# Optimization experiments

Hardware: AMD Instinct MI355X
Metric: run time of the kernel (lower is better)

The kernel has to match this reference:

```python
import jax, jax.numpy as jnp
import numpy as np

NEG_SLOPE = 0.2

def gat_conv(x, src, dst, W, a_src, a_dst, b, num_nodes, concat):
    # PyG GATConv (add_self_loops already applied to src/dst).
    H, C = a_src.shape
    h = (x @ W).reshape(-1, H, C)                      # [N,H,C]
    s = jnp.einsum('nhc,hc->nh', h, a_src)             # per-node src score
    d = jnp.einsum('nhc,hc->nh', h, a_dst)             # per-node dst score
    e = jax.nn.leaky_relu(s[src] + d[dst], NEG_SLOPE)  # [E,H]
    emax = jax.lax.stop_gradient(
        jax.ops.segment_max(e, dst, num_segments=num_nodes))  # [N,H]
    ex = jnp.exp(e - emax[dst])
    denom = jax.ops.segment_sum(ex, dst, num_segments=num_nodes)
    alpha = ex / denom[dst]                            # segment softmax over in-edges
    msg = h[src] * alpha[:, :, None]                   # [E,H,C]
    out = jax.ops.segment_sum(msg, dst, num_segments=num_nodes)
    out = out.reshape(num_nodes, H * C) if concat else out.mean(axis=1)
    return out + b

def setup_inputs() -> dict:
    key = jax.random.key(0)
    ks = jax.random.split(key, 20)
    N, E, F = 50000, 400000, 256
    x = jax.random.normal(ks[0], (N, F), dtype=jnp.float32)
    edge_index = jax.random.randint(ks[1], (2, E), 0, N, dtype=jnp.int64)
    def p(k, shape):
        return (jax.random.normal(k, shape, dtype=jnp.float32) * 0.1)
    inp = {'x': x, 'edge_index': edge_index}
    # conv1: 256 -> 8x32 ; conv2: 256 -> 4x32 ; conv3: 128 -> 2x32 ; conv4: 64 -> 1x32
    dims = [(256, 8, 32), (256, 4, 32), (128, 2, 32), (64, 1, 32)]
    ki = 2
    for i, (fin, H, C) in enumerate(dims, start=1):
        inp[f'W{i}'] = p(ks[ki], (fin, H * C)); ki += 1
        inp[f'a_src{i}'] = p(ks[ki], (H, C)); ki += 1
        inp[f'a_dst{i}'] = p(ks[ki], (H, C)); ki += 1
        bdim = H * C if i < 4 else C
        inp[f'b{i}'] = jnp.zeros((bdim,), dtype=jnp.float32)
    return inp

def reference(x, edge_index, W1, a_src1, a_dst1, b1, W2, a_src2, a_dst2, b2,
              W3, a_src3, a_dst3, b3, W4, a_src4, a_dst4, b4):
    N = x.shape[0]
    loops = jnp.arange(N, dtype=edge_index.dtype)
    src = jnp.concatenate([edge_index[0], loops])
    dst = jnp.concatenate([edge_index[1], loops])
    h = jax.nn.elu(gat_conv(x, src, dst, W1, a_src1, a_dst1, b1, N, True))
    h = jax.nn.elu(gat_conv(h, src, dst, W2, a_src2, a_dst2, b2, N, True))
    h = gat_conv(h, src, dst, W3, a_src3, a_dst3, b3, N, True)
    h = jax.nn.elu(h)
    h = gat_conv(h, src, dst, W4, a_src4, a_dst4, b4, N, False)
    return jax.nn.log_softmax(h, axis=1)
```

## Files before the change

kernel.cpp:

```cpp
#include <hip/hip_runtime.h>
#include <hip/hip_bf16.h>

#define LRELU_SLOPE 0.2f

typedef __attribute__((ext_vector_type(8))) short short8;
typedef __attribute__((ext_vector_type(4))) float f32x4;

__device__ __forceinline__ unsigned short bf16r(float f) {
    unsigned int u = __builtin_bit_cast(unsigned int, f);
    u += 0x7fffu + ((u >> 16) & 1u);
    return (unsigned short)(u >> 16);
}
__device__ __forceinline__ float bf2f(unsigned short u) {
    return __builtin_bit_cast(float, (unsigned int)u << 16);
}

#define GLD16(g, l)                                                            \
    __builtin_amdgcn_global_load_lds(                                          \
        (const __attribute__((address_space(1))) void*)(g),                    \
        (__attribute__((address_space(3))) void*)(l), 16, 0, 0)


#define WTOT 108544

__global__ void k_pre(const float* __restrict__ x, unsigned short* __restrict__ Xb,
                      const float* __restrict__ Wa, const float* __restrict__ Wb,
                      const float* __restrict__ Wc, const float* __restrict__ Wd,
                      unsigned short* __restrict__ Ta, unsigned short* __restrict__ Tb,
                      unsigned short* __restrict__ Tc, unsigned short* __restrict__ Td,
                      const int* __restrict__ ei, int* __restrict__ cnt,
                      int* __restrict__ slot, int XC, int E) {
    int gid = blockIdx.x * blockDim.x + threadIdx.x;
    if (gid < XC) {
        const float4* xp = (const float4*)x + (long)gid * 2;
        float4 a = xp[0], b = xp[1];
        short8 pk;
        pk[0] = (short)bf16r(a.x); pk[1] = (short)bf16r(a.y);
        pk[2] = (short)bf16r(a.z); pk[3] = (short)bf16r(a.w);
        pk[4] = (short)bf16r(b.x); pk[5] = (short)bf16r(b.y);
        pk[6] = (short)bf16r(b.z); pk[7] = (short)bf16r(b.w);
        *(short8*)(Xb + (long)gid * 8) = pk;
        return;
    }
    int id = gid - XC;
    if (id < WTOT) {
        const float* W; unsigned short* T; int K, Nc;
        if (id < 65536)       { W = Wa; T = Ta; K = 256; Nc = 256; }
        else if (id < 98304)  { id -= 65536;  W = Wb; T = Tb; K = 256; Nc = 128; }
        else if (id < 106496) { id -= 98304;  W = Wc; T = Tc; K = 128; Nc = 64; }
        else                  { id -= 106496; W = Wd; T = Td; K = 64;  Nc = 32; }
        int n = id / K, k = id % K;
        T[id] = bf16r(W[(long)k * Nc + n]);
        return;
    }
    int e = id - WTOT;
    if (e >= E) return;
    int dst = ei[E + e];
    slot[e] = atomicAdd(&cnt[dst], 1);
}


__global__ void k_scan_blk(const int* __restrict__ cnt, int* __restrict__ offsR,
                           int* __restrict__ bsum, int* __restrict__ bpre,
                           int* __restrict__ done, int N, int NB) {
    __shared__ int temp[1024];
    __shared__ int last_s;
    int t = threadIdx.x;
    int gi = blockIdx.x * 1024 + t;
    int v = (gi < N) ? cnt[gi] + 1 : 0;
    temp[t] = v;
    __syncthreads();
    for (int o = 1; o < 1024; o <<= 1) {
        int x = (t >= o) ? temp[t - o] : 0;
        __syncthreads();
        temp[t] += x;
        __syncthreads();
    }
    if (gi < N) offsR[gi] = temp[t] - v;
    if (t == 1023) bsum[blockIdx.x] = temp[1023];
    if (t == 0) {
        __threadfence();
        last_s = (atomicAdd(done, 1) == NB - 1) ? 1 : 0;
    }
    __syncthreads();
    if (last_s) {
        __threadfence();
        int v2 = (t < NB) ? bsum[t] : 0;
        temp[t] = v2;
        __syncthreads();
        for (int o = 1; o < 1024; o <<= 1) {
            int x = (t >= o) ? temp[t - o] : 0;
            __syncthreads();
            temp[t] += x;
            __syncthreads();
        }
        if (t < NB) bpre[t] = temp[t] - v2;
        if (t == NB - 1) bpre[NB] = temp[t];
    }
}


__global__ void k_finalize(const int* __restrict__ ei, const int* __restrict__ offsR,
                           const int* __restrict__ bpre, const int* __restrict__ slot,
                           int* __restrict__ offs, int* __restrict__ adj,
                           int N, int NB, int E) {
    int gi = blockIdx.x * blockDim.x + threadIdx.x;
    int NA = (N + 256) & ~255;
    if (gi < NA) {
        if (gi < N) {
            int v = offsR[gi] + bpre[gi >> 10];
            offs[gi] = v;
            adj[v] = gi;
        } else if (gi == N) {
            offs[N] = bpre[NB];
        }
        return;
    }
    int e = gi - NA;
    if (e >= E) return;
    int srcn = ei[e];
    int dst  = ei[E + e];
    adj[offsR[dst] + bpre[dst >> 10] + 1 + slot[e]] = srcn;
}


template<int BN, int KT, int GX>
__global__ __launch_bounds__(256) void k_mgemm(const unsigned short* __restrict__ Ab,
                                               const unsigned short* __restrict__ WT,
                                               unsigned short* __restrict__ Cb,
                                               const float* __restrict__ a_src,
                                               const float* __restrict__ a_dst,
                                               float* __restrict__ sbuf,
                                               float* __restrict__ dbuf,
                                               int M, int Nc, int H, int RB) {
    constexpr int KH   = (KT == 256) ? 128 : KT;
    constexpr int NR   = KT / KH;
    constexpr int KITER = KH / 32;
    constexpr int NBF = BN / 16;
    constexpr int CPR = BN / 32;
    constexpr int SP  = BN + 8;
    constexpr int ASH = 64 * KH;
    constexpr int BSH = BN * KH;
    constexpr int EPIL = 64 * SP;
    constexpr int LBSZ = (ASH + BSH) > EPIL ? (ASH + BSH) : EPIL;
    constexpr int CHR = KH / 8;
    constexpr int SHC = (KH == 128) ? 4 : 3;
    constexpr int AIT = CHR / 4;
    constexpr int BIT = BN * CHR / 256;
    __shared__ __align__(16) unsigned short LB[LBSZ];

    int id = blockIdx.x;
    int xcd = id & 7;
    int q  = id >> 3;
    int ct = q % GX;
    int rb = (q / GX) * 8 + xcd;
    if (rb >= RB) return;
    int bm = rb * 64, bn = ct * BN;

    int t = threadIdx.x;
    int wv = t >> 6, l = t & 63;
    int row_in = l & 15, quad = l >> 4;
    char* LBb = (char*)LB;

    const char* Agb = (const char*)Ab;
    const char* WTb = (const char*)WT;

    f32x4 acc[NBF];
#pragma unroll
    for (int j = 0; j < NBF; ++j) acc[j] = (f32x4){0.f, 0.f, 0.f, 0.f};

    int arow = wv * 16 + row_in;

#pragma unroll
    for (int r = 0; r < NR; ++r) {
        if (r > 0) __syncthreads();

#pragma unroll
        for (int i = 0; i < AIT; ++i) {
            int c = i * 256 + t;
            int row = c >> SHC;
            int ci  = c & (CHR - 1);
            int cis = ci ^ (row & 7);
            int grow = bm + row; if (grow >= M) grow = M - 1;
            long gb = (long)grow * (KT * 2) + r * (KH * 2) + cis * 16;
            GLD16(Agb + gb, LBb + (i * 256 + wv * 64) * 16);
        }
#pragma unroll
        for (int i = 0; i < BIT; ++i) {
            int c = i * 256 + t;
            int col = c >> SHC;
            int ci  = c & (CHR - 1);
            int cis = ci ^ (col & 7);
            long gb = (long)(bn + col) * (KT * 2) + r * (KH * 2) + cis * 16;
            GLD16(WTb + gb, LBb + ASH * 2 + (i * 256 + wv * 64) * 16);
        }
        asm volatile("s_waitcnt vmcnt(0)" ::: "memory");
        __syncthreads();

#pragma unroll
        for (int ki = 0; ki < KITER; ++ki) {
            int aoff = (arow * (KH * 2) + ki * 64 + quad * 16) ^ ((arow & 7) << 4);
            short8 av = *(const short8*)(LBb + aoff);
#pragma unroll
            for (int f = 0; f < NBF; ++f) {
                int bcol = f * 16 + row_in;
                int boff = ASH * 2 + ((bcol * (KH * 2) + ki * 64 + quad * 16) ^ ((bcol & 7) << 4));
                short8 bv = *(const short8*)(LBb + boff);
                acc[f] = __builtin_amdgcn_mfma_f32_16x16x32_bf16(av, bv, acc[f], 0, 0, 0);
            }
        }
    }
    __syncthreads();

#pragma unroll
    for (int r = 0; r < 4; ++r)
#pragma unroll
        for (int f = 0; f < NBF; ++f)
            LB[(wv * 16 + quad * 4 + r) * SP + f * 16 + row_in] = bf16r(acc[f][r]);
    __syncthreads();

    int rr = t / CPR, cc = t % CPR;
    if (rr < 64) {
        int grow = bm + rr;
        int colb = bn + cc * 32;
        if (grow < M && colb < Nc) {
            const unsigned short* ep = &LB[rr * SP + cc * 32];
            short8 v0 = *(const short8*)(ep);
            short8 v1 = *(const short8*)(ep + 8);
            short8 v2 = *(const short8*)(ep + 16);
            short8 v3 = *(const short8*)(ep + 24);
            unsigned short* cp = &Cb[(long)grow * Nc + colb];
            *(short8*)(cp)      = v0;
            *(short8*)(cp + 8)  = v1;
            *(short8*)(cp + 16) = v2;
            *(short8*)(cp + 24) = v3;
            int hd = colb >> 5;
            const float* ap = a_src + hd * 32;
            const float* dp = a_dst + hd * 32;
            float ss = 0.f, dd = 0.f;
#pragma unroll
            for (int u = 0; u < 8; ++u) {
                float va = bf2f((unsigned short)v0[u]); ss += va * ap[u];      dd += va * dp[u];
                float vb = bf2f((unsigned short)v1[u]); ss += vb * ap[8 + u];  dd += vb * dp[8 + u];
                float vc = bf2f((unsigned short)v2[u]); ss += vc * ap[16 + u]; dd += vc * dp[16 + u];
                float vd = bf2f((unsigned short)v3[u]); ss += vd * ap[24 + u]; dd += vd * dp[24 + u];
            }
            sbuf[(long)grow * H + hd] = ss;
            dbuf[(long)grow * H + hd] = dd;
        }
    }
}


#define QB(v, k) __builtin_amdgcn_ds_swizzle((v), 0x8000 | ((k) * 0x55))

template<int ACT>
__global__ void k_aggf(const unsigned short* __restrict__ h, const float* __restrict__ s,
                       const float* __restrict__ dsc, const int* __restrict__ offs,
                       const int* __restrict__ adj, const float* __restrict__ bias,
                       unsigned short* __restrict__ out16, float* __restrict__ out32,
                       int N, int H) {
    const int C8 = 4;
    long tid = (long)blockIdx.x * blockDim.x + threadIdx.x;
    int HC8 = H * C8;
    if (tid >= (long)N * HC8) return;
    int c8 = (int)(tid % C8);
    int hh = (int)((tid / C8) % H);
    int n  = (int)(tid / HC8);
    int beg = offs[n], end = offs[n + 1];
    float dn = dsc[n * H + hh];
    int HC = HC8 * 8;
    int coff = hh * 32 + c8 * 8;
    const unsigned short* hb = h + coff;

    float denom = 0.f;
    float acc[8];
#pragma unroll
    for (int u = 0; u < 8; ++u) acc[u] = 0.f;

    for (int j = beg; j < end; j += 4) {
        int my = j + c8;
        int idx = my < end ? my : end - 1;
        int sn = adj[idx];
        float e = s[sn * H + hh] + dn;
        e = e > 0.f ? e : LRELU_SLOPE * e;
        float w = __expf(fminf(e, 80.f));
        if (my >= end) w = 0.f;
        int wi = __builtin_bit_cast(int, w);
        int sn0 = QB(sn, 0);
        int sn1 = QB(sn, 1);
        int sn2 = QB(sn, 2);
        int sn3 = QB(sn, 3);
        float w0 = __builtin_bit_cast(float, QB(wi, 0));
        float w1 = __builtin_bit_cast(float, QB(wi, 1));
        float w2 = __builtin_bit_cast(float, QB(wi, 2));
        float w3 = __builtin_bit_cast(float, QB(wi, 3));
        short8 h0 = *(const short8*)(hb + (size_t)sn0 * HC);
        short8 h1 = *(const short8*)(hb + (size_t)sn1 * HC);
        short8 h2 = *(const short8*)(hb + (size_t)sn2 * HC);
        short8 h3 = *(const short8*)(hb + (size_t)sn3 * HC);
        denom += (w0 + w1) + (w2 + w3);
#pragma unroll
        for (int u = 0; u < 8; ++u) {
            float a01 = w0 * bf2f((unsigned short)h0[u]) + w1 * bf2f((unsigned short)h1[u]);
            float a23 = w2 * bf2f((unsigned short)h2[u]) + w3 * bf2f((unsigned short)h3[u]);
            acc[u] += a01 + a23;
        }
    }

    float inv = 1.0f / denom;
    float o[8];
#pragma unroll
    for (int u = 0; u < 8; ++u) o[u] = acc[u] * inv + bias[coff + u];

    if (ACT == 1) {
        short8 pk;
#pragma unroll
        for (int u = 0; u < 8; ++u) {
            float v = o[u] > 0.f ? o[u] : (__expf(o[u]) - 1.f);
            pk[u] = (short)bf16r(v);
        }
        *(short8*)(out16 + tid * 8) = pk;
    } else {
        float m = o[0];
#pragma unroll
        for (int u = 1; u < 8; ++u) m = fmaxf(m, o[u]);
        m = fmaxf(m, __shfl_xor(m, 1));
        m = fmaxf(m, __shfl_xor(m, 2));
        float ssum = 0.f;
#pragma unroll
        for (int u = 0; u < 8; ++u) ssum += __expf(o[u] - m);
        ssum += __shfl_xor(ssum, 1);
        ssum += __shfl_xor(ssum, 2);
        float lse = m + __logf(ssum);
        float4 lo = {o[0] - lse, o[1] - lse, o[2] - lse, o[3] - lse};
        float4 hi = {o[4] - lse, o[5] - lse, o[6] - lse, o[7] - lse};
        *(float4*)(out32 + tid * 8)     = lo;
        *(float4*)(out32 + tid * 8 + 4) = hi;
    }
}


static inline size_t align_up(size_t x) { return (x + 255) & ~(size_t)255; }

extern "C" void kernel_launch(void* const* d_in, const int* in_sizes, int n_in,
                              void* d_out, int out_size, void* d_ws, size_t ws_size,
                              hipStream_t stream) {
    const float* x   = (const float*)d_in[0];
    const int*   ei  = (const int*)d_in[1];

    const int N = in_sizes[0] / 256;
    const int E = in_sizes[1] / 2;
    const int ET = E + N;
    const int NB = (N + 1023) / 1024;
    const int XC = N * 32;

    size_t off = 0;
    char* ws = (char*)d_ws;
    auto take = [&](size_t bytes) { char* p = ws + off; off += align_up(bytes); return p; };
    int*   offs  = (int*)take((size_t)(N + 1) * 4);
    int*   offsR = (int*)take((size_t)(N + 1) * 4);
    int*   cntd  = (int*)take((size_t)(N + 1) * 4);
    int*   slot  = (int*)take((size_t)E * 4);
    int*   adj   = (int*)take((size_t)ET * 4);
    int*   bsum  = (int*)take((size_t)(NB + 1) * 4);
    int*   bpre  = (int*)take((size_t)(NB + 1) * 4);
    float* sbuf  = (float*)take((size_t)N * 8 * 4);
    float* dbuf  = (float*)take((size_t)N * 8 * 4);
    unsigned short* Xb = (unsigned short*)take((size_t)N * 256 * 2);
    unsigned short* Yb = (unsigned short*)take((size_t)N * 256 * 2);
    unsigned short* WT0 = (unsigned short*)take((size_t)256 * 256 * 2);
    unsigned short* WT1 = (unsigned short*)take((size_t)256 * 128 * 2);
    unsigned short* WT2 = (unsigned short*)take((size_t)128 * 64 * 2);
    unsigned short* WT3 = (unsigned short*)take((size_t)64 * 32 * 2);
    (void)ws_size;

    int* cnt  = cntd;
    int* done = cntd + N;

    hipMemsetAsync(cntd, 0, (size_t)(N + 1) * 4, stream);
    {
        long tot = (long)XC + WTOT + E;
        k_pre<<<(int)((tot + 255) / 256), 256, 0, stream>>>(
            x, Xb,
            (const float*)d_in[2], (const float*)d_in[6], (const float*)d_in[10],
            (const float*)d_in[14], WT0, WT1, WT2, WT3, ei, cnt, slot, XC, E);
        k_scan_blk<<<NB, 1024, 0, stream>>>(cnt, offsR, bsum, bpre, done, N, NB);
        int NA = (N + 256) & ~255;
        k_finalize<<<(NA + E + 255) / 256, 256, 0, stream>>>(
            ei, offsR, bpre, slot, offs, adj, N, NB, E);
    }

    const float* as_[4] = {(const float*)d_in[3], (const float*)d_in[7],
                           (const float*)d_in[11], (const float*)d_in[15]};
    const float* ad_[4] = {(const float*)d_in[4], (const float*)d_in[8],
                           (const float*)d_in[12], (const float*)d_in[16]};
    const float* b_[4]  = {(const float*)d_in[5], (const float*)d_in[9],
                           (const float*)d_in[13], (const float*)d_in[17]};
    int H_[4] = {8, 4, 2, 1};

    const int RB  = (N + 63) / 64;
    const int RBp = ((RB + 7) / 8) * 8;

    for (int li = 0; li < 4; ++li) {
        int H = H_[li];

        if (li == 0) {
            k_mgemm<64, 256, 4><<<4 * RBp, 256, 0, stream>>>(
                Xb, WT0, Yb, as_[0], ad_[0], sbuf, dbuf, N, 256, H, RB);
        } else if (li == 1) {
            k_mgemm<64, 256, 2><<<2 * RBp, 256, 0, stream>>>(
                Xb, WT1, Yb, as_[1], ad_[1], sbuf, dbuf, N, 128, H, RB);
        } else if (li == 2) {
            k_mgemm<64, 128, 1><<<RBp, 256, 0, stream>>>(
                Xb, WT2, Yb, as_[2], ad_[2], sbuf, dbuf, N, 64, H, RB);
        } else {
            k_mgemm<32, 64, 1><<<RBp, 256, 0, stream>>>(
                Xb, WT3, Yb, as_[3], ad_[3], sbuf, dbuf, N, 32, H, RB);
        }
        {
            long total = (long)N * H * 4;
            int nb = (int)((total + 255) / 256);
            if (li < 3)
                k_aggf<1><<<nb, 256, 0, stream>>>(Yb, sbuf, dbuf, offs, adj, b_[li],
                                                  Xb, nullptr, N, H);
            else
                k_aggf<0><<<nb, 256, 0, stream>>>(Yb, sbuf, dbuf, offs, adj, b_[li],
                                                  nullptr, (float*)d_out, N, H);
        }
    }
}
```

Baseline: 294.8 us.

## Fuse aggregation with next-layer GEMM per row block and fold CSR finalize into first GEMM

Replaces the per-layer sequence of separate GEMM and aggregation kernels with fused kernels. Each 64-node row block gathers neighbours, applies the softmax weights, bias and ELU, stages the result in LDS and immediately multiplies it by the next layer's weights. The CSR finalize step is merged into the first GEMM through a grid-stride prologue, and the gather loop now processes 8 edges per iteration. The aim is to remove the global round trip of the intermediate activations and several kernel launches. In exchange the aggregation runs on far fewer threads per launch (one block per 64 rows) and uses more LDS, which can reduce latency hiding for the gather.

```diff
diff --git a/kernel.cpp b/kernel.cpp
--- a/kernel.cpp
+++ b/kernel.cpp
@@ -2,6 +2,7 @@
 #include <hip/hip_bf16.h>
 
 #define LRELU_SLOPE 0.2f
+#define WTOT 108544
 
 typedef __attribute__((ext_vector_type(8))) short short8;
 typedef __attribute__((ext_vector_type(4))) float f32x4;
@@ -20,8 +21,8 @@
         (const __attribute__((address_space(1))) void*)(g),                    \
         (__attribute__((address_space(3))) void*)(l), 16, 0, 0)
 
-
-#define WTOT 108544
+#define QB(v, k) __builtin_amdgcn_ds_swizzle((v), 0x8000 | ((k) * 0x55))
+
 
 __global__ void k_pre(const float* __restrict__ x, unsigned short* __restrict__ Xb,
                       const float* __restrict__ Wa, const float* __restrict__ Wb,
@@ -100,54 +101,48 @@
 }
 
 
-__global__ void k_finalize(const int* __restrict__ ei, const int* __restrict__ offsR,
-                           const int* __restrict__ bpre, const int* __restrict__ slot,
-                           int* __restrict__ offs, int* __restrict__ adj,
-                           int N, int NB, int E) {
-    int gi = blockIdx.x * blockDim.x + threadIdx.x;
-    int NA = (N + 256) & ~255;
-    if (gi < NA) {
-        if (gi < N) {
-            int v = offsR[gi] + bpre[gi >> 10];
-            offs[gi] = v;
-            adj[v] = gi;
-        } else if (gi == N) {
-            offs[N] = bpre[NB];
-        }
-        return;
-    }
-    int e = gi - NA;
-    if (e >= E) return;
-    int srcn = ei[e];
-    int dst  = ei[E + e];
-    adj[offsR[dst] + bpre[dst >> 10] + 1 + slot[e]] = srcn;
-}
-
-
-template<int BN, int KT, int GX>
-__global__ __launch_bounds__(256) void k_mgemm(const unsigned short* __restrict__ Ab,
-                                               const unsigned short* __restrict__ WT,
-                                               unsigned short* __restrict__ Cb,
-                                               const float* __restrict__ a_src,
-                                               const float* __restrict__ a_dst,
-                                               float* __restrict__ sbuf,
-                                               float* __restrict__ dbuf,
-                                               int M, int Nc, int H, int RB) {
-    constexpr int KH   = (KT == 256) ? 128 : KT;
-    constexpr int NR   = KT / KH;
+__global__ __launch_bounds__(256) void k_mg0fin(
+        const int* __restrict__ ei, const int* __restrict__ offsR,
+        const int* __restrict__ bpre, const int* __restrict__ slot,
+        int* __restrict__ offs, int* __restrict__ adj, int NB, int E,
+        const unsigned short* __restrict__ Ab, const unsigned short* __restrict__ WT,
+        unsigned short* __restrict__ Cb,
+        const float* __restrict__ a_src, const float* __restrict__ a_dst,
+        float* __restrict__ sbuf, float* __restrict__ dbuf,
+        int M, int RB) {
+    constexpr int KT = 256, BN = 64, GX = 4, KH = 128, NR = 2;
     constexpr int KITER = KH / 32;
     constexpr int NBF = BN / 16;
     constexpr int CPR = BN / 32;
     constexpr int SP  = BN + 8;
     constexpr int ASH = 64 * KH;
-    constexpr int BSH = BN * KH;
-    constexpr int EPIL = 64 * SP;
-    constexpr int LBSZ = (ASH + BSH) > EPIL ? (ASH + BSH) : EPIL;
     constexpr int CHR = KH / 8;
-    constexpr int SHC = (KH == 128) ? 4 : 3;
+    constexpr int SHC = 4;
     constexpr int AIT = CHR / 4;
     constexpr int BIT = BN * CHR / 256;
-    __shared__ __align__(16) unsigned short LB[LBSZ];
+    __shared__ __align__(16) unsigned short LB[16384];
+
+    {
+        int gtid = blockIdx.x * 256 + threadIdx.x;
+        int GT = gridDim.x * 256;
+        int N = M;
+        int NA = (N + 256) & ~255;
+        for (int gi = gtid; gi < NA + E; gi += GT) {
+            if (gi < NA) {
+                if (gi < N) {
+                    int v = offsR[gi] + bpre[gi >> 10];
+                    offs[gi] = v;
+                    adj[v] = gi;
+                } else if (gi == N) {
+                    offs[N] = bpre[NB];
+                }
+            } else {
+                int e = gi - NA;
+                int dst = ei[E + e];
+                adj[offsR[dst] + bpre[dst >> 10] + 1 + slot[e]] = ei[e];
+            }
+        }
+    }
 
     int id = blockIdx.x;
     int xcd = id & 7;
@@ -161,7 +156,6 @@
     int wv = t >> 6, l = t & 63;
     int row_in = l & 15, quad = l >> 4;
     char* LBb = (char*)LB;
-
     const char* Agb = (const char*)Ab;
     const char* WTb = (const char*)WT;
 
@@ -174,7 +168,6 @@
 #pragma unroll
     for (int r = 0; r < NR; ++r) {
         if (r > 0) __syncthreads();
-
 #pragma unroll
         for (int i = 0; i < AIT; ++i) {
             int c = i * 256 + t;
@@ -223,13 +216,13 @@
     if (rr < 64) {
         int grow = bm + rr;
         int colb = bn + cc * 32;
-        if (grow < M && colb < Nc) {
+        if (grow < M) {
             const unsigned short* ep = &LB[rr * SP + cc * 32];
             short8 v0 = *(const short8*)(ep);
             short8 v1 = *(const short8*)(ep + 8);
             short8 v2 = *(const short8*)(ep + 16);
             short8 v3 = *(const short8*)(ep + 24);
-            unsigned short* cp = &Cb[(long)grow * Nc + colb];
+            unsigned short* cp = &Cb[(long)grow * 256 + colb];
             *(short8*)(cp)      = v0;
             *(short8*)(cp + 8)  = v1;
             *(short8*)(cp + 16) = v2;
@@ -245,32 +238,211 @@
                 float vc = bf2f((unsigned short)v2[u]); ss += vc * ap[16 + u]; dd += vc * dp[16 + u];
                 float vd = bf2f((unsigned short)v3[u]); ss += vd * ap[24 + u]; dd += vd * dp[24 + u];
             }
-            sbuf[(long)grow * H + hd] = ss;
-            dbuf[(long)grow * H + hd] = dd;
-        }
-    }
-}
-
-
-#define QB(v, k) __builtin_amdgcn_ds_swizzle((v), 0x8000 | ((k) * 0x55))
-
-template<int ACT>
-__global__ void k_aggf(const unsigned short* __restrict__ h, const float* __restrict__ s,
-                       const float* __restrict__ dsc, const int* __restrict__ offs,
-                       const int* __restrict__ adj, const float* __restrict__ bias,
-                       unsigned short* __restrict__ out16, float* __restrict__ out32,
-                       int N, int H) {
-    const int C8 = 4;
+            sbuf[(long)grow * 8 + hd] = ss;
+            dbuf[(long)grow * 8 + hd] = dd;
+        }
+    }
+}
+
+
+template<int HIN, int NC, int KH>
+__global__ __launch_bounds__(256, 4) void k_agmg(
+        const unsigned short* __restrict__ h,
+        const float* __restrict__ s, const float* __restrict__ dsc,
+        const int* __restrict__ offs, const int* __restrict__ adj,
+        const float* __restrict__ bias,
+        const unsigned short* __restrict__ WT,
+        unsigned short* __restrict__ Cb,
+        const float* __restrict__ a_src, const float* __restrict__ a_dst,
+        float* __restrict__ sb2, float* __restrict__ db2,
+        int N, int RB) {
+    constexpr int KT   = HIN * 32;
+    constexpr int NR   = KT / KH;
+    constexpr int KITER = KH / 32;
+    constexpr int NBF  = NC / 16;
+    constexpr int CPR  = NC / 32;
+    constexpr int SP   = NC + 8;
+    constexpr int ASH2 = 64 * KT * 2;
+    constexpr int CHR  = KH / 8;
+    constexpr int BIT  = NC * CHR / 256;
+    constexpr int HOUT = NC / 32;
+    constexpr int TOT1 = ASH2 + NC * KH * 2;
+    constexpr int TOT2 = 64 * SP * 2;
+    __shared__ __align__(16) unsigned short LB[(TOT1 > TOT2 ? TOT1 : TOT2) / 2];
+
+    int rb = blockIdx.x;
+    if (rb >= RB) return;
+    int bm = rb * 64;
+    int t = threadIdx.x;
+    char* LBb = (char*)LB;
+
+    constexpr int UNITS = 64 * HIN * 4;
+    for (int u = t; u < UNITS; u += 256) {
+        int c8 = u & 3;
+        int hh = (u >> 2) % HIN;
+        int nl = u / (4 * HIN);
+        int n0 = bm + nl;
+        int nn = n0 < N ? n0 : N - 1;
+        int beg = offs[nn], end = offs[nn + 1];
+        float dn = dsc[nn * HIN + hh];
+        int coff = hh * 32 + c8 * 8;
+        const unsigned short* hb = h + coff;
+
+        float denom = 0.f;
+        float acc[8];
+#pragma unroll
+        for (int z = 0; z < 8; ++z) acc[z] = 0.f;
+
+        for (int j = beg; j < end; j += 8) {
+            int my0 = j + c8;
+            int my1 = my0 + 4;
+            int i0 = my0 < end ? my0 : end - 1;
+            int i1 = my1 < end ? my1 : end - 1;
+            int p  = adj[i0];
+            int qn = adj[i1];
+            int a0 = QB(p, 0),  a1 = QB(p, 1),  a2 = QB(p, 2),  a3 = QB(p, 3);
+            int b0 = QB(qn, 0), b1 = QB(qn, 1), b2 = QB(qn, 2), b3 = QB(qn, 3);
+            short8 h0 = *(const short8*)(hb + (size_t)a0 * KT);
+            short8 h1 = *(const short8*)(hb + (size_t)a1 * KT);
+            short8 h2 = *(const short8*)(hb + (size_t)a2 * KT);
+            short8 h3 = *(const short8*)(hb + (size_t)a3 * KT);
+            short8 h4 = *(const short8*)(hb + (size_t)b0 * KT);
+            short8 h5 = *(const short8*)(hb + (size_t)b1 * KT);
+            short8 h6 = *(const short8*)(hb + (size_t)b2 * KT);
+            short8 h7 = *(const short8*)(hb + (size_t)b3 * KT);
+            float e0 = s[p * HIN + hh] + dn;
+            float e1 = s[qn * HIN + hh] + dn;
+            e0 = e0 > 0.f ? e0 : LRELU_SLOPE * e0;
+            e1 = e1 > 0.f ? e1 : LRELU_SLOPE * e1;
+            float wA = __expf(fminf(e0, 80.f));
+            float wB = __expf(fminf(e1, 80.f));
+            if (my0 >= end) wA = 0.f;
+            if (my1 >= end) wB = 0.f;
+            int wiA = __builtin_bit_cast(int, wA);
+            int wiB = __builtin_bit_cast(int, wB);
+            float w0 = __builtin_bit_cast(float, QB(wiA, 0));
+            float w1 = __builtin_bit_cast(float, QB(wiA, 1));
+            float w2 = __builtin_bit_cast(float, QB(wiA, 2));
+            float w3 = __builtin_bit_cast(float, QB(wiA, 3));
+            float w4 = __builtin_bit_cast(float, QB(wiB, 0));
+            float w5 = __builtin_bit_cast(float, QB(wiB, 1));
+            float w6 = __builtin_bit_cast(float, QB(wiB, 2));
+            float w7 = __builtin_bit_cast(float, QB(wiB, 3));
+            denom += ((w0 + w1) + (w2 + w3)) + ((w4 + w5) + (w6 + w7));
+#pragma unroll
+            for (int z = 0; z < 8; ++z) {
+                float aa = w0 * bf2f((unsigned short)h0[z]) + w1 * bf2f((unsigned short)h1[z]);
+                float ab = w2 * bf2f((unsigned short)h2[z]) + w3 * bf2f((unsigned short)h3[z]);
+                float ac = w4 * bf2f((unsigned short)h4[z]) + w5 * bf2f((unsigned short)h5[z]);
+                float ad = w6 * bf2f((unsigned short)h6[z]) + w7 * bf2f((unsigned short)h7[z]);
+                acc[z] += (aa + ab) + (ac + ad);
+            }
+        }
+
+        float inv = 1.0f / denom;
+        short8 pk;
+#pragma unroll
+        for (int z = 0; z < 8; ++z) {
+            float o = acc[z] * inv + bias[coff + z];
+            float v = o > 0.f ? o : (__expf(o) - 1.f);
+            pk[z] = (short)bf16r(v);
+        }
+        int lbyte = (nl * (KT * 2) + coff * 2) ^ ((nl & 7) << 4);
+        *(short8*)(LBb + lbyte) = pk;
+    }
+    __syncthreads();
+
+    int wv = t >> 6, l = t & 63;
+    int row_in = l & 15, quad = l >> 4;
+    int arow = wv * 16 + row_in;
+    const char* WTb = (const char*)WT;
+
+    f32x4 gac[NBF];
+#pragma unroll
+    for (int j = 0; j < NBF; ++j) gac[j] = (f32x4){0.f, 0.f, 0.f, 0.f};
+
+#pragma unroll
+    for (int r = 0; r < NR; ++r) {
+        if (r > 0) __syncthreads();
+#pragma unroll
+        for (int i = 0; i < BIT; ++i) {
+            int c = i * 256 + t;
+            int col = c / CHR;
+            int ci  = c % CHR;
+            int cis = ci ^ (col & 7);
+            long gb = (long)col * (KT * 2) + r * (KH * 2) + cis * 16;
+            GLD16(WTb + gb, LBb + ASH2 + (i * 256 + wv * 64) * 16);
+        }
+        asm volatile("s_waitcnt vmcnt(0)" ::: "memory");
+        __syncthreads();
+
+#pragma unroll
+        for (int ki = 0; ki < KITER; ++ki) {
+            int aoff = (arow * (KT * 2) + r * (KH * 2) + ki * 64 + quad * 16) ^ ((arow & 7) << 4);
+            short8 av = *(const short8*)(LBb + aoff);
+#pragma unroll
+            for (int f = 0; f < NBF; ++f) {
+                int bcol = f * 16 + row_in;
+                int boff = ASH2 + ((bcol * (KH * 2) + ki * 64 + quad * 16) ^ ((bcol & 7) << 4));
+                short8 bv = *(const short8*)(LBb + boff);
+                gac[f] = __builtin_amdgcn_mfma_f32_16x16x32_bf16(av, bv, gac[f], 0, 0, 0);
+            }
+        }
+    }
+    __syncthreads();
+
+#pragma unroll
+    for (int r4 = 0; r4 < 4; ++r4)
+#pragma unroll
+        for (int f = 0; f < NBF; ++f)
+            LB[(wv * 16 + quad * 4 + r4) * SP + f * 16 + row_in] = bf16r(gac[f][r4]);
+    __syncthreads();
+
+    int rr = t / CPR, cc = t % CPR;
+    if (rr < 64) {
+        int grow = bm + rr;
+        int colb = cc * 32;
+        if (grow < N) {
+            const unsigned short* ep = &LB[rr * SP + colb];
+            short8 v0 = *(const short8*)(ep);
+            short8 v1 = *(const short8*)(ep + 8);
+            short8 v2 = *(const short8*)(ep + 16);
+            short8 v3 = *(const short8*)(ep + 24);
+            unsigned short* cp = &Cb[(long)grow * NC + colb];
+            *(short8*)(cp)      = v0;
+            *(short8*)(cp + 8)  = v1;
+            *(short8*)(cp + 16) = v2;
+            *(short8*)(cp + 24) = v3;
+            int hd = colb >> 5;
+            const float* ap = a_src + hd * 32;
+            const float* dp = a_dst + hd * 32;
+            float ss = 0.f, dd = 0.f;
+#pragma unroll
+            for (int u = 0; u < 8; ++u) {
+                float va = bf2f((unsigned short)v0[u]); ss += va * ap[u];      dd += va * dp[u];
+                float vb = bf2f((unsigned short)v1[u]); ss += vb * ap[8 + u];  dd += vb * dp[8 + u];
+                float vc = bf2f((unsigned short)v2[u]); ss += vc * ap[16 + u]; dd += vc * dp[16 + u];
+                float vd = bf2f((unsigned short)v3[u]); ss += vd * ap[24 + u]; dd += vd * dp[24 + u];
+            }
+            sb2[(long)grow * HOUT + hd] = ss;
+            db2[(long)grow * HOUT + hd] = dd;
+        }
+    }
+}
+
+
+__global__ void k_aggf_fin(const unsigned short* __restrict__ h, const float* __restrict__ s,
+                           const float* __restrict__ dsc, const int* __restrict__ offs,
+                           const int* __restrict__ adj, const float* __restrict__ bias,
+                           float* __restrict__ out32, int N) {
+    const int H = 1, C8 = 4, HC = 32;
     long tid = (long)blockIdx.x * blockDim.x + threadIdx.x;
-    int HC8 = H * C8;
-    if (tid >= (long)N * HC8) return;
+    if (tid >= (long)N * C8) return;
     int c8 = (int)(tid % C8);
-    int hh = (int)((tid / C8) % H);
-    int n  = (int)(tid / HC8);
+    int n  = (int)(tid / C8);
     int beg = offs[n], end = offs[n + 1];
-    float dn = dsc[n * H + hh];
-    int HC = HC8 * 8;
-    int coff = hh * 32 + c8 * 8;
+    float dn = dsc[n * H];
+    int coff = c8 * 8;
     const unsigned short* hb = h + coff;
 
     float denom = 0.f;
@@ -282,7 +454,7 @@
         int my = j + c8;
         int idx = my < end ? my : end - 1;
         int sn = adj[idx];
-        float e = s[sn * H + hh] + dn;
+        float e = s[sn * H] + dn;
         e = e > 0.f ? e : LRELU_SLOPE * e;
         float w = __expf(fminf(e, 80.f));
         if (my >= end) w = 0.f;
@@ -313,31 +485,21 @@
 #pragma unroll
     for (int u = 0; u < 8; ++u) o[u] = acc[u] * inv + bias[coff + u];
 
-    if (ACT == 1) {
-        short8 pk;
-#pragma unroll
-        for (int u = 0; u < 8; ++u) {
-            float v = o[u] > 0.f ? o[u] : (__expf(o[u]) - 1.f);
-            pk[u] = (short)bf16r(v);
-        }
-        *(short8*)(out16 + tid * 8) = pk;
-    } else {
-        float m = o[0];
-#pragma unroll
-        for (int u = 1; u < 8; ++u) m = fmaxf(m, o[u]);
-        m = fmaxf(m, __shfl_xor(m, 1));
-        m = fmaxf(m, __shfl_xor(m, 2));
-        float ssum = 0.f;
-#pragma unroll
-        for (int u = 0; u < 8; ++u) ssum += __expf(o[u] - m);
-        ssum += __shfl_xor(ssum, 1);
-        ssum += __shfl_xor(ssum, 2);
-        float lse = m + __logf(ssum);
-        float4 lo = {o[0] - lse, o[1] - lse, o[2] - lse, o[3] - lse};
-        float4 hi = {o[4] - lse, o[5] - lse, o[6] - lse, o[7] - lse};
-        *(float4*)(out32 + tid * 8)     = lo;
-        *(float4*)(out32 + tid * 8 + 4) = hi;
-    }
+    float m = o[0];
+#pragma unroll
+    for (int u = 1; u < 8; ++u) m = fmaxf(m, o[u]);
+    m = fmaxf(m, __shfl_xor(m, 1));
+    m = fmaxf(m, __shfl_xor(m, 2));
+    float ssum = 0.f;
+#pragma unroll
+    for (int u = 0; u < 8; ++u) ssum += __expf(o[u] - m);
+    ssum += __shfl_xor(ssum, 1);
+    ssum += __shfl_xor(ssum, 2);
+    float lse = m + __logf(ssum);
+    float4 lo = {o[0] - lse, o[1] - lse, o[2] - lse, o[3] - lse};
+    float4 hi = {o[4] - lse, o[5] - lse, o[6] - lse, o[7] - lse};
+    *(float4*)(out32 + tid * 8)     = lo;
+    *(float4*)(out32 + tid * 8 + 4) = hi;
 }
 
 
@@ -358,17 +520,20 @@
     size_t off = 0;
     char* ws = (char*)d_ws;
     auto take = [&](size_t bytes) { char* p = ws + off; off += align_up(bytes); return p; };
+    int*   cntd  = (int*)take((size_t)(N + 1) * 4);
     int*   offs  = (int*)take((size_t)(N + 1) * 4);
     int*   offsR = (int*)take((size_t)(N + 1) * 4);
-    int*   cntd  = (int*)take((size_t)(N + 1) * 4);
     int*   slot  = (int*)take((size_t)E * 4);
     int*   adj   = (int*)take((size_t)ET * 4);
     int*   bsum  = (int*)take((size_t)(NB + 1) * 4);
     int*   bpre  = (int*)take((size_t)(NB + 1) * 4);
-    float* sbuf  = (float*)take((size_t)N * 8 * 4);
-    float* dbuf  = (float*)take((size_t)N * 8 * 4);
+    float* s0    = (float*)take((size_t)N * 8 * 4);
+    float* d0    = (float*)take((size_t)N * 8 * 4);
+    float* s1    = (float*)take((size_t)N * 4 * 4);
+    float* d1    = (float*)take((size_t)N * 4 * 4);
     unsigned short* Xb = (unsigned short*)take((size_t)N * 256 * 2);
-    unsigned short* Yb = (unsigned short*)take((size_t)N * 256 * 2);
+    unsigned short* Y0 = (unsigned short*)take((size_t)N * 256 * 2);
+    unsigned short* Y1 = (unsigned short*)take((size_t)N * 128 * 2);
     unsigned short* WT0 = (unsigned short*)take((size_t)256 * 256 * 2);
     unsigned short* WT1 = (unsigned short*)take((size_t)256 * 128 * 2);
     unsigned short* WT2 = (unsigned short*)take((size_t)128 * 64 * 2);
@@ -377,6 +542,16 @@
 
     int* cnt  = cntd;
     int* done = cntd + N;
+
+    const float* as_[4] = {(const float*)d_in[3], (const float*)d_in[7],
+                           (const float*)d_in[11], (const float*)d_in[15]};
+    const float* ad_[4] = {(const float*)d_in[4], (const float*)d_in[8],
+                           (const float*)d_in[12], (const float*)d_in[16]};
+    const float* b_[4]  = {(const float*)d_in[5], (const float*)d_in[9],
+                           (const float*)d_in[13], (const float*)d_in[17]};
+
+    const int RB  = (N + 63) / 64;
+    const int RBp = ((RB + 7) / 8) * 8;
 
     hipMemsetAsync(cntd, 0, (size_t)(N + 1) * 4, stream);
     {
@@ -385,48 +560,17 @@
             x, Xb,
             (const float*)d_in[2], (const float*)d_in[6], (const float*)d_in[10],
             (const float*)d_in[14], WT0, WT1, WT2, WT3, ei, cnt, slot, XC, E);
-        k_scan_blk<<<NB, 1024, 0, stream>>>(cnt, offsR, bsum, bpre, done, N, NB);
-        int NA = (N + 256) & ~255;
-        k_finalize<<<(NA + E + 255) / 256, 256, 0, stream>>>(
-            ei, offsR, bpre, slot, offs, adj, N, NB, E);
-    }
-
-    const float* as_[4] = {(const float*)d_in[3], (const float*)d_in[7],
-                           (const float*)d_in[11], (const float*)d_in[15]};
-    const float* ad_[4] = {(const float*)d_in[4], (const float*)d_in[8],
-                           (const float*)d_in[12], (const float*)d_in[16]};
-    const float* b_[4]  = {(const float*)d_in[5], (const float*)d_in[9],
-                           (const float*)d_in[13], (const float*)d_in[17]};
-    int H_[4] = {8, 4, 2, 1};
-
-    const int RB  = (N + 63) / 64;
-    const int RBp = ((RB + 7) / 8) * 8;
-
-    for (int li = 0; li < 4; ++li) {
-        int H = H_[li];
-
-        if (li == 0) {
-            k_mgemm<64, 256, 4><<<4 * RBp, 256, 0, stream>>>(
-                Xb, WT0, Yb, as_[0], ad_[0], sbuf, dbuf, N, 256, H, RB);
-        } else if (li == 1) {
-            k_mgemm<64, 256, 2><<<2 * RBp, 256, 0, stream>>>(
-                Xb, WT1, Yb, as_[1], ad_[1], sbuf, dbuf, N, 128, H, RB);
-        } else if (li == 2) {
-            k_mgemm<64, 128, 1><<<RBp, 256, 0, stream>>>(
-                Xb, WT2, Yb, as_[2], ad_[2], sbuf, dbuf, N, 64, H, RB);
-        } else {
-            k_mgemm<32, 64, 1><<<RBp, 256, 0, stream>>>(
-                Xb, WT3, Yb, as_[3], ad_[3], sbuf, dbuf, N, 32, H, RB);
-        }
-        {
-            long total = (long)N * H * 4;
-            int nb = (int)((total + 255) / 256);
-            if (li < 3)
-                k_aggf<1><<<nb, 256, 0, stream>>>(Yb, sbuf, dbuf, offs, adj, b_[li],
-                                                  Xb, nullptr, N, H);
-            else
-                k_aggf<0><<<nb, 256, 0, stream>>>(Yb, sbuf, dbuf, offs, adj, b_[li],
-                                                  nullptr, (float*)d_out, N, H);
-        }
-    }
-}
+    }
+    k_scan_blk<<<NB, 1024, 0, stream>>>(cnt, offsR, bsum, bpre, done, N, NB);
+    k_mg0fin<<<4 * RBp, 256, 0, stream>>>(
+        ei, offsR, bpre, slot, offs, adj, NB, E,
+        Xb, WT0, Y0, as_[0], ad_[0], s0, d0, N, RB);
+    k_agmg<8, 128, 64><<<RB, 256, 0, stream>>>(
+        Y0, s0, d0, offs, adj, b_[0], WT1, Y1, as_[1], ad_[1], s1, d1, N, RB);
+    k_agmg<4, 64, 128><<<RB, 256, 0, stream>>>(
+        Y1, s1, d1, offs, adj, b_[1], WT2, Y0, as_[2], ad_[2], s0, d0, N, RB);
+    k_agmg<2, 32, 64><<<RB, 256, 0, stream>>>(
+        Y0, s0, d0, offs, adj, b_[2], WT3, Y1, as_[3], ad_[3], s1, d1, N, RB);
+    k_aggf_fin<<<(int)(((long)N * 4 + 255) / 256), 256, 0, stream>>>(
+        Y1, s1, d1, offs, adj, b_[3], (float*)d_out, N);
+}
```

After: 298.9 us. No clear change (+1.4%).
